# Optimization experiments

Measured on AMD Instinct MI355X. Metric: run time of the kernel, lower is better.

Reference implementation:

```python
import jax, jax.numpy as jnp
import numpy as np

B, L, D, H = 2, 2048, 1024, 16
HD = D // H  # head dim = 64


def setup_inputs() -> dict:
    key = jax.random.key(0)
    ks = jax.random.split(key, 5)
    s = 1.0 / np.sqrt(D)
    return {
        "x": jax.random.normal(ks[0], (B, L, D), dtype=jnp.float32),
        "mask": jnp.ones((B, 1, 1, L), dtype=jnp.int32),
        "Wq": jax.random.normal(ks[1], (D, D), dtype=jnp.float32) * s,
        "bq": jnp.zeros((D,), dtype=jnp.float32),
        "Wk": jax.random.normal(ks[2], (D, D), dtype=jnp.float32) * s,
        "bk": jnp.zeros((D,), dtype=jnp.float32),
        "Wv": jax.random.normal(ks[3], (D, D), dtype=jnp.float32) * s,
        "bv": jnp.zeros((D,), dtype=jnp.float32),
        "Wo": jax.random.normal(ks[4], (D, D), dtype=jnp.float32) * s,
        "bo": jnp.zeros((D,), dtype=jnp.float32),
    }


def reference(x, mask, Wq, bq, Wk, bk, Wv, bv, Wo, bo):
    Bx, Lx = x.shape[0], x.shape[1]
    # torch nn.Linear: y = x @ W.T + b
    q = (jnp.einsum("bld,ed->ble", x, Wq) + bq).reshape(Bx, Lx, H, HD).transpose(0, 2, 1, 3)
    k = (jnp.einsum("bld,ed->ble", x, Wk) + bk).reshape(Bx, Lx, H, HD).transpose(0, 2, 1, 3)
    v = (jnp.einsum("bld,ed->ble", x, Wv) + bv).reshape(Bx, Lx, H, HD).transpose(0, 2, 1, 3)
    # [B, H, L, L] scores
    scores = jnp.einsum("bhqd,bhkd->bhqk", q, k) / np.sqrt(HD).astype(np.float32)
    # faithful to original: masked positions are set to the tiny value 1e-9 (not -inf)
    scores = jnp.where(mask == 0, jnp.float32(1e-9), scores)
    attn = jax.nn.softmax(scores, axis=-1)
    # dropout_prob=0.0 -> identity (eval mode)
    out = jnp.einsum("bhqk,bhkd->bhqd", attn, v)  # [B, H, L, HD]
    out = out.transpose(0, 2, 1, 3).reshape(Bx, Lx, D)
    return jnp.einsum("bld,ed->ble", out, Wo) + bo
```

## Files before the change

kernel.cpp:

```cpp
#include <hip/hip_runtime.h>
#include <hip/hip_bf16.h>

typedef _Float16 f16;
typedef _Float16 f16x8 __attribute__((ext_vector_type(8)));
typedef _Float16 f16x4 __attribute__((ext_vector_type(4)));
typedef float f32x4 __attribute__((ext_vector_type(4)));
typedef int i32x4 __attribute__((ext_vector_type(4)));

#define LDS_LOAD16(gptr, lptr)                                                             \
  __builtin_amdgcn_global_load_lds(                                                        \
      (const __attribute__((address_space(1))) unsigned int*)(gptr),                       \
      (__attribute__((address_space(3))) unsigned int*)(lptr), 16, 0, 0)

#define ALPHA 0.18033688f
#define MASKVAL 1.44269504e-9f

__global__ __launch_bounds__(256) void conv_all(const float* __restrict__ x,
                                                const float* __restrict__ Wq,
                                                const float* __restrict__ Wk,
                                                const float* __restrict__ Wv,
                                                const float* __restrict__ Wo,
                                                f16* __restrict__ xh, f16* __restrict__ wqh,
                                                f16* __restrict__ wkh, f16* __restrict__ wvh,
                                                f16* __restrict__ woh) {
  int i = blockIdx.x * 256 + threadIdx.x;
  const float* src;
  f16* dst;
  int off;
  if (i < 524288) {
    src = x; dst = xh; off = i;
  } else {
    int j = i - 524288;
    int w = j >> 17;
    off = j & 131071;
    src = (w == 0) ? Wq : (w == 1) ? Wk : (w == 2) ? Wv : Wo;
    dst = (w == 0) ? wqh : (w == 1) ? wkh : (w == 2) ? wvh : woh;
  }
  const float4* s4 = (const float4*)src;
  float4 a = s4[2 * off];
  float4 b = s4[2 * off + 1];
  f16x8 o = {(f16)a.x, (f16)a.y, (f16)a.z, (f16)a.w,
             (f16)b.x, (f16)b.y, (f16)b.z, (f16)b.w};
  *(f16x8*)(dst + (size_t)off * 8) = o;
}

__global__ __launch_bounds__(256) void gemm_qkv(const f16* __restrict__ A,
                                                const f16* __restrict__ W0,
                                                const f16* __restrict__ W1,
                                                const f16* __restrict__ W2,
                                                const float* __restrict__ b0,
                                                const float* __restrict__ b1,
                                                const float* __restrict__ b2,
                                                f16* __restrict__ qo, f16* __restrict__ ko,
                                                f16* __restrict__ vo) {
  constexpr int K = 1024, BM = 128, BK = 32, NKT = K / BK;
  __shared__ f16 aT[2][BM * BK];
  __shared__ f16 bT[2][BM * BK];
  const int rid = (blockIdx.x & 7) * 96 + (blockIdx.x >> 3);
  const int z = rid >> 8;
  const f16* Bw = (z == 0) ? W0 : (z == 1) ? W1 : W2;
  const float* bias = (z == 0) ? b0 : (z == 1) ? b1 : b2;
  const int tid = threadIdx.x, wid = tid >> 6, lane = tid & 63;
  const int mb = ((rid >> 3) & 31) * BM, nb = (rid & 7) * BM;
  const int wr = wid >> 1, wc = wid & 1;
  const int lr = lane & 15, hi = lane >> 4;

  f32x4 acc[4][4] = {};

  const int r0 = tid >> 2, s0 = tid & 3;
  const int ci1 = 256 + tid, r1 = ci1 >> 2, s1 = ci1 & 3;

#define STAGE_QKV(bb, kt)                                                                   \
  do {                                                                                      \
    const int kb_ = (kt) * BK;                                                              \
    LDS_LOAD16(A + (size_t)(mb + r0) * K + kb_ + s0 * 8, (char*)aT[bb] + wid * 1024);       \
    LDS_LOAD16(Bw + (size_t)(nb + r0) * K + kb_ + s0 * 8, (char*)bT[bb] + wid * 1024);      \
    LDS_LOAD16(A + (size_t)(mb + r1) * K + kb_ + s1 * 8, (char*)aT[bb] + 4096 + wid * 1024);\
    LDS_LOAD16(Bw + (size_t)(nb + r1) * K + kb_ + s1 * 8, (char*)bT[bb] + 4096 + wid * 1024);\
  } while (0)

  STAGE_QKV(0, 0);
  for (int kt = 0; kt < NKT; ++kt) {
    const int p = kt & 1;
    if (kt + 1 < NKT) {
      STAGE_QKV(p ^ 1, kt + 1);
      asm volatile("s_waitcnt vmcnt(4)" ::: "memory");
    } else {
      asm volatile("s_waitcnt vmcnt(0)" ::: "memory");
    }
    __builtin_amdgcn_s_barrier();

    f16x8 af[4], bf[4];
#pragma unroll
    for (int i = 0; i < 4; ++i) af[i] = *(const f16x8*)&aT[p][(wr * 64 + i * 16 + lr) * BK + hi * 8];
#pragma unroll
    for (int j = 0; j < 4; ++j) bf[j] = *(const f16x8*)&bT[p][(wc * 64 + j * 16 + lr) * BK + hi * 8];
    __builtin_amdgcn_s_setprio(1);
#pragma unroll
    for (int i = 0; i < 4; ++i)
#pragma unroll
      for (int j = 0; j < 4; ++j)
        acc[i][j] = __builtin_amdgcn_mfma_f32_16x16x32_f16(af[i], bf[j], acc[i][j], 0, 0, 0);
    __builtin_amdgcn_s_setprio(0);
    __builtin_amdgcn_s_barrier();
  }

  const float scale = (z == 0) ? ALPHA : 1.0f;
#pragma unroll
  for (int i = 0; i < 4; ++i) {
#pragma unroll
    for (int j = 0; j < 4; ++j) {
      const int row = mb + wr * 64 + i * 16 + hi * 4;
      const int col = nb + wc * 64 + j * 16 + lr;
      const float bv = bias[col];
      const int hh = col >> 6, dd = col & 63;
      if (z == 2) {
        const int bb = row >> 11, l = row & 2047;
        f16x4 v4;
#pragma unroll
        for (int r = 0; r < 4; ++r) v4[r] = (f16)(acc[i][j][r] + bv);
        *(f16x4*)(vo + ((((size_t)bb * 16 + hh) * 64 + dd) * 2048 + l)) = v4;
      } else {
        f16* o = z ? ko : qo;
#pragma unroll
        for (int r = 0; r < 4; ++r) {
          const int m2 = row + r;
          const int bb = m2 >> 11, l = m2 & 2047;
          o[((((size_t)bb * 16 + hh) * 2048 + l) * 64) + dd] = (f16)((acc[i][j][r] + bv) * scale);
        }
      }
    }
  }
}

__global__ __launch_bounds__(256) void gemm_o(const f16* __restrict__ A,
                                              const f16* __restrict__ W,
                                              const float* __restrict__ bias,
                                              float* __restrict__ out) {
  constexpr int K = 1024, N = 1024, BK = 32, NKT = K / BK;
  __shared__ f16 aT[2][64 * BK];
  __shared__ f16 bT[2][128 * BK];
  const int rid = (blockIdx.x & 7) * 64 + (blockIdx.x >> 3);
  const int tid = threadIdx.x, wid = tid >> 6, lane = tid & 63;
  const int lr = lane & 15, hi = lane >> 4;
  const int mb = (rid >> 3) * 64, nb = (rid & 7) * 128;
  const int wr = wid >> 1, wc = wid & 1;
  f32x4 acc[2][4] = {};
  const int ra = tid >> 2, sa = tid & 3;
  const int rb1 = (256 + tid) >> 2, sb1 = (256 + tid) & 3;

#define STAGE_O(bb, kt)                                                                     \
  do {                                                                                      \
    const int kb_ = (kt) * BK;                                                              \
    LDS_LOAD16(A + (size_t)(mb + ra) * K + kb_ + sa * 8, (char*)aT[bb] + wid * 1024);       \
    LDS_LOAD16(W + (size_t)(nb + ra) * K + kb_ + sa * 8, (char*)bT[bb] + wid * 1024);       \
    LDS_LOAD16(W + (size_t)(nb + rb1) * K + kb_ + sb1 * 8, (char*)bT[bb] + 4096 + wid * 1024);\
  } while (0)

  STAGE_O(0, 0);
  for (int kt = 0; kt < NKT; ++kt) {
    const int p = kt & 1;
    if (kt + 1 < NKT) {
      STAGE_O(p ^ 1, kt + 1);
      asm volatile("s_waitcnt vmcnt(3)" ::: "memory");
    } else {
      asm volatile("s_waitcnt vmcnt(0)" ::: "memory");
    }
    __builtin_amdgcn_s_barrier();
    f16x8 af[2], bf[4];
#pragma unroll
    for (int i = 0; i < 2; ++i) af[i] = *(const f16x8*)&aT[p][(wr * 32 + i * 16 + lr) * BK + hi * 8];
#pragma unroll
    for (int j = 0; j < 4; ++j) bf[j] = *(const f16x8*)&bT[p][(wc * 64 + j * 16 + lr) * BK + hi * 8];
    __builtin_amdgcn_s_setprio(1);
#pragma unroll
    for (int i = 0; i < 2; ++i)
#pragma unroll
      for (int j = 0; j < 4; ++j)
        acc[i][j] = __builtin_amdgcn_mfma_f32_16x16x32_f16(af[i], bf[j], acc[i][j], 0, 0, 0);
    __builtin_amdgcn_s_setprio(0);
    __builtin_amdgcn_s_barrier();
  }
#pragma unroll
  for (int i = 0; i < 2; ++i)
#pragma unroll
    for (int j = 0; j < 4; ++j) {
      const int col = nb + wc * 64 + j * 16 + lr;
      const float bv = bias[col];
#pragma unroll
      for (int r = 0; r < 4; ++r)
        out[(size_t)(mb + wr * 32 + i * 16 + hi * 4 + r) * N + col] = acc[i][j][r] + bv;
    }
}

__global__ __launch_bounds__(256, 4) void attn4w(const f16* __restrict__ Qh,
                                                 const f16* __restrict__ Kh,
                                                 const f16* __restrict__ Vt,
                                                 const int* __restrict__ mask,
                                                 f16* __restrict__ Oa) {
  constexpr int L = 2048, HD = 64, H = 16, NT = L / 64;
  __shared__ __align__(16) char ldsb[32768];

  const int tid = threadIdx.x, w = tid >> 6, lane = tid & 63;
  const int lr = lane & 15, hi = lane >> 4;
  const int sw = lr & 7;

  const int bid = blockIdx.x;
  const int head = (bid & 7) * 4 + (bid >> 8);
  const int qb = (bid >> 3) & 31;
  const int b = head >> 4, h = head & 15;
  const int qr0 = qb * 64 + w * 16;

  const f16* Qb = Qh + (size_t)head * L * HD;
  const f16* Kb = Kh + (size_t)head * L * HD;
  const f16* Vb = Vt + (size_t)head * HD * L;
  const int* mrow = mask + b * L;

  int mred = 1;
  {
    const int4* m4 = (const int4*)mrow;
#pragma unroll
    for (int j = 0; j < 8; ++j) {
      int4 v = m4[lane + j * 64];
      mred &= v.x & v.y & v.z & v.w;
    }
  }
  const bool allm = __all(mred == 1);

  const int srow = lane >> 3;
  const int schk = (lane & 7) ^ srow;

#define STAGE4W(bb, kt)                                                                     \
  _Pragma("unroll") for (int c = 0; c < 2; ++c) {                                           \
    LDS_LOAD16(Kb + (size_t)((kt) * 64 + w * 16 + c * 8 + srow) * HD + schk * 8,            \
               ldsb + (bb) * 16384 + w * 2048 + c * 1024);                                  \
    LDS_LOAD16(Vb + (size_t)(w * 16 + c * 8 + srow) * L + (kt) * 64 + schk * 8,             \
               ldsb + (bb) * 16384 + 8192 + w * 2048 + c * 1024);                           \
  }

  const char* kbase0 = ldsb + lr * 128 + ((hi ^ sw) * 16);
  const char* kbase1 = ldsb + lr * 128 + (((4 + hi) ^ sw) * 16);

  f16x8 qf[2];
#pragma unroll
  for (int k2 = 0; k2 < 2; ++k2)
    qf[k2] = *(const f16x8*)&Qb[(size_t)(qr0 + lr) * HD + k2 * 32 + hi * 8];

  f32x4 oacc[4] = {};
  f32x4 lacc = {};
  const f32x4 zacc = {0.f, 0.f, 0.f, 0.f};
  const f16x8 ones = {1, 1, 1, 1, 1, 1, 1, 1};

  int4 mvA[4], mvB[4];
  if (!allm) {
#pragma unroll
    for (int nf = 0; nf < 4; ++nf) mvA[nf] = *(const int4*)&mrow[nf * 16 + hi * 4];
  }
  STAGE4W(0, 0);

#define ATTN_ITER(kt, P, MVR, MVL)                                                          \
  do {                                                                                      \
    asm volatile("s_waitcnt vmcnt(0)" ::: "memory");                                        \
    __builtin_amdgcn_s_barrier();                                                           \
    if ((kt) + 1 < NT) {                                                                    \
      if (!allm) {                                                                          \
        _Pragma("unroll") for (int nf = 0; nf < 4; ++nf)                                    \
            MVL[nf] = *(const int4*)&mrow[((kt) + 1) * 64 + nf * 16 + hi * 4];              \
      }                                                                                     \
      STAGE4W((P) ^ 1, (kt) + 1);                                                           \
    }                                                                                       \
    f16x8 kf[4][2];                                                                         \
    _Pragma("unroll") for (int nf = 0; nf < 4; ++nf) {                                      \
      kf[nf][0] = *(const f16x8*)(kbase0 + (P) * 16384 + nf * 2048);                        \
      kf[nf][1] = *(const f16x8*)(kbase1 + (P) * 16384 + nf * 2048);                        \
    }                                                                                       \
    f32x4 s[4];                                                                             \
    __builtin_amdgcn_s_setprio(1);                                                          \
    _Pragma("unroll") for (int nf = 0; nf < 4; ++nf) {                                      \
      f32x4 z = __builtin_amdgcn_mfma_f32_16x16x32_f16(kf[nf][0], qf[0], zacc, 0, 0, 0);    \
      s[nf] = __builtin_amdgcn_mfma_f32_16x16x32_f16(kf[nf][1], qf[1], z, 0, 0, 0);         \
    }                                                                                       \
    __builtin_amdgcn_s_setprio(0);                                                          \
    int wpk[4][2];                                                                          \
    _Pragma("unroll") for (int nf = 0; nf < 4; ++nf) {                                      \
      float p0, p1, p2, p3;                                                                 \
      if (allm) {                                                                           \
        p0 = __builtin_amdgcn_exp2f(s[nf][0]);                                              \
        p1 = __builtin_amdgcn_exp2f(s[nf][1]);                                              \
        p2 = __builtin_amdgcn_exp2f(s[nf][2]);                                              \
        p3 = __builtin_amdgcn_exp2f(s[nf][3]);                                              \
      } else {                                                                              \
        p0 = __builtin_amdgcn_exp2f(MVR[nf].x ? s[nf][0] : MASKVAL);                        \
        p1 = __builtin_amdgcn_exp2f(MVR[nf].y ? s[nf][1] : MASKVAL);                        \
        p2 = __builtin_amdgcn_exp2f(MVR[nf].z ? s[nf][2] : MASKVAL);                        \
        p3 = __builtin_amdgcn_exp2f(MVR[nf].w ? s[nf][3] : MASKVAL);                        \
      }                                                                                     \
      wpk[nf][0] = __builtin_bit_cast(int, __builtin_amdgcn_cvt_pkrtz(p0, p1));             \
      wpk[nf][1] = __builtin_bit_cast(int, __builtin_amdgcn_cvt_pkrtz(p2, p3));             \
    }                                                                                       \
    f16x8 pf[2];                                                                            \
    _Pragma("unroll") for (int k2 = 0; k2 < 2; ++k2) {                                      \
      int A0 = wpk[2 * k2][0], B0 = wpk[2 * k2 + 1][0];                                     \
      int A1 = wpk[2 * k2][1], B1 = wpk[2 * k2 + 1][1];                                     \
      asm("v_permlane32_swap_b32 %0, %1" : "+v"(A0), "+v"(B0));                             \
      asm("v_permlane16_swap_b32 %0, %1" : "+v"(A0), "+v"(B0));                             \
      asm("v_permlane32_swap_b32 %0, %1" : "+v"(A1), "+v"(B1));                             \
      asm("v_permlane16_swap_b32 %0, %1" : "+v"(A1), "+v"(B1));                             \
      i32x4 cc = {A0, A1, B0, B1};                                                          \
      pf[k2] = __builtin_bit_cast(f16x8, cc);                                               \
    }                                                                                       \
    __builtin_amdgcn_s_setprio(1);                                                          \
    _Pragma("unroll") for (int k2 = 0; k2 < 2; ++k2) {                                      \
      const char* vbase = (k2 ? kbase1 : kbase0) + (P) * 16384 + 8192;                      \
      _Pragma("unroll") for (int df = 0; df < 4; ++df) {                                    \
        f16x8 vf = *(const f16x8*)(vbase + df * 2048);                                      \
        oacc[df] = __builtin_amdgcn_mfma_f32_16x16x32_f16(pf[k2], vf, oacc[df], 0, 0, 0);   \
      }                                                                                     \
      lacc = __builtin_amdgcn_mfma_f32_16x16x32_f16(pf[k2], ones, lacc, 0, 0, 0);           \
    }                                                                                       \
    __builtin_amdgcn_s_setprio(0);                                                          \
  } while (0)

  for (int kt = 0; kt < NT; kt += 2) {
    ATTN_ITER(kt, 0, mvA, mvB);
    ATTN_ITER(kt + 1, 1, mvB, mvA);
  }

  f32x4 rinv;
#pragma unroll
  for (int r = 0; r < 4; ++r) rinv[r] = 1.0f / lacc[r];
#pragma unroll
  for (int df = 0; df < 4; ++df)
#pragma unroll
    for (int r = 0; r < 4; ++r) {
      const int l = qr0 + hi * 4 + r;
      Oa[(((size_t)b * L + l) * H + h) * HD + df * 16 + lr] = (f16)(oacc[df][r] * rinv[r]);
    }
}

extern "C" void kernel_launch(void* const* d_in, const int* in_sizes, int n_in,
                              void* d_out, int out_size, void* d_ws, size_t ws_size,
                              hipStream_t stream) {
  const float* x  = (const float*)d_in[0];
  const int* mask = (const int*)d_in[1];
  const float* Wq = (const float*)d_in[2];
  const float* bq = (const float*)d_in[3];
  const float* Wk = (const float*)d_in[4];
  const float* bk = (const float*)d_in[5];
  const float* Wv = (const float*)d_in[6];
  const float* bv = (const float*)d_in[7];
  const float* Wo = (const float*)d_in[8];
  const float* bo = (const float*)d_in[9];
  float* out = (float*)d_out;

  char* ws = (char*)d_ws;
  const size_t MB = 1u << 20;
  f16* xh  = (f16*)(ws);
  f16* wqh = (f16*)(ws + 8 * MB);
  f16* wkh = (f16*)(ws + 10 * MB);
  f16* wvh = (f16*)(ws + 12 * MB);
  f16* woh = (f16*)(ws + 14 * MB);
  f16* qh  = (f16*)(ws + 16 * MB);
  f16* kh  = (f16*)(ws + 24 * MB);
  f16* vth = (f16*)(ws + 32 * MB);
  f16* oah = (f16*)(ws + 40 * MB);

  conv_all<<<4096, 256, 0, stream>>>(x, Wq, Wk, Wv, Wo, xh, wqh, wkh, wvh, woh);

  gemm_qkv<<<768, 256, 0, stream>>>(xh, wqh, wkh, wvh, bq, bk, bv, qh, kh, vth);

  attn4w<<<dim3(1024), 256, 0, stream>>>(qh, kh, vth, mask, oah);

  gemm_o<<<512, 256, 0, stream>>>(oah, woh, bo, out);
}
```

Baseline: 117.3 us.

## Switch attention to 32x32x16 MFMA with 32 query rows per wave

The attention kernel now uses 32x32x16 MFMA tiles with 32 query rows per wave and 128 per block, halving the grid to 512 blocks. Each K/V LDS tile is reused across twice as many query rows, so there is half as much staging traffic per query. The row sum is now accumulated with scalar adds plus one cross-lane shuffle instead of an extra ones-MFMA, and fewer permlane swaps are needed. The costs are more registers (launch bounds drop to 2 blocks per SM) and fewer blocks, which may hurt occupancy and latency hiding.

```diff
diff --git a/kernel.cpp b/kernel.cpp
--- a/kernel.cpp
+++ b/kernel.cpp
@@ -5,6 +5,7 @@
 typedef _Float16 f16x8 __attribute__((ext_vector_type(8)));
 typedef _Float16 f16x4 __attribute__((ext_vector_type(4)));
 typedef float f32x4 __attribute__((ext_vector_type(4)));
+typedef float f32x16 __attribute__((ext_vector_type(16)));
 typedef int i32x4 __attribute__((ext_vector_type(4)));
 
 #define LDS_LOAD16(gptr, lptr)                                                             \
@@ -193,23 +194,22 @@
     }
 }
 
-__global__ __launch_bounds__(256, 4) void attn4w(const f16* __restrict__ Qh,
-                                                 const f16* __restrict__ Kh,
-                                                 const f16* __restrict__ Vt,
-                                                 const int* __restrict__ mask,
-                                                 f16* __restrict__ Oa) {
+__global__ __launch_bounds__(256, 2) void attn32q(const f16* __restrict__ Qh,
+                                                  const f16* __restrict__ Kh,
+                                                  const f16* __restrict__ Vt,
+                                                  const int* __restrict__ mask,
+                                                  f16* __restrict__ Oa) {
   constexpr int L = 2048, HD = 64, H = 16, NT = L / 64;
   __shared__ __align__(16) char ldsb[32768];
 
   const int tid = threadIdx.x, w = tid >> 6, lane = tid & 63;
-  const int lr = lane & 15, hi = lane >> 4;
-  const int sw = lr & 7;
+  const int q32 = lane & 31, h5 = lane >> 5, x7 = lane & 7;
 
   const int bid = blockIdx.x;
-  const int head = (bid & 7) * 4 + (bid >> 8);
-  const int qb = (bid >> 3) & 31;
+  const int head = (bid & 7) * 4 + (bid >> 7);
+  const int qb = (bid >> 3) & 15;
   const int b = head >> 4, h = head & 15;
-  const int qr0 = qb * 64 + w * 16;
+  const int qr0 = qb * 128 + w * 32;
 
   const f16* Qb = Qh + (size_t)head * L * HD;
   const f16* Kb = Kh + (size_t)head * L * HD;
@@ -230,7 +230,7 @@
   const int srow = lane >> 3;
   const int schk = (lane & 7) ^ srow;
 
-#define STAGE4W(bb, kt)                                                                     \
+#define STAGE32(bb, kt)                                                                     \
   _Pragma("unroll") for (int c = 0; c < 2; ++c) {                                           \
     LDS_LOAD16(Kb + (size_t)((kt) * 64 + w * 16 + c * 8 + srow) * HD + schk * 8,            \
                ldsb + (bb) * 16384 + w * 2048 + c * 1024);                                  \
@@ -238,103 +238,103 @@
                ldsb + (bb) * 16384 + 8192 + w * 2048 + c * 1024);                           \
   }
 
-  const char* kbase0 = ldsb + lr * 128 + ((hi ^ sw) * 16);
-  const char* kbase1 = ldsb + lr * 128 + (((4 + hi) ^ sw) * 16);
-
-  f16x8 qf[2];
-#pragma unroll
-  for (int k2 = 0; k2 < 2; ++k2)
-    qf[k2] = *(const f16x8*)&Qb[(size_t)(qr0 + lr) * HD + k2 * 32 + hi * 8];
-
-  f32x4 oacc[4] = {};
-  f32x4 lacc = {};
-  const f32x4 zacc = {0.f, 0.f, 0.f, 0.f};
-  const f16x8 ones = {1, 1, 1, 1, 1, 1, 1, 1};
-
-  int4 mvA[4], mvB[4];
+  const char* kb[4];
+#pragma unroll
+  for (int s = 0; s < 4; ++s)
+    kb[s] = ldsb + q32 * 128 + (((2 * s + h5) ^ x7) * 16);
+
+  f16x8 qf[4];
+#pragma unroll
+  for (int s = 0; s < 4; ++s)
+    qf[s] = *(const f16x8*)&Qb[(size_t)(qr0 + q32) * HD + s * 16 + h5 * 8];
+
+  f32x16 oacc[2] = {};
+  float lsum = 0.f;
+  const f32x16 zacc = {};
+
+  int4 mvA[2][4], mvB[2][4];
   if (!allm) {
 #pragma unroll
-    for (int nf = 0; nf < 4; ++nf) mvA[nf] = *(const int4*)&mrow[nf * 16 + hi * 4];
-  }
-  STAGE4W(0, 0);
-
-#define ATTN_ITER(kt, P, MVR, MVL)                                                          \
+    for (int t = 0; t < 2; ++t)
+#pragma unroll
+      for (int g = 0; g < 4; ++g) mvA[t][g] = *(const int4*)&mrow[t * 32 + 4 * h5 + 8 * g];
+  }
+  STAGE32(0, 0);
+
+#define ATTN_I32(kt, P, MVR, MVL)                                                           \
   do {                                                                                      \
     asm volatile("s_waitcnt vmcnt(0)" ::: "memory");                                        \
     __builtin_amdgcn_s_barrier();                                                           \
     if ((kt) + 1 < NT) {                                                                    \
       if (!allm) {                                                                          \
-        _Pragma("unroll") for (int nf = 0; nf < 4; ++nf)                                    \
-            MVL[nf] = *(const int4*)&mrow[((kt) + 1) * 64 + nf * 16 + hi * 4];              \
+        _Pragma("unroll") for (int t = 0; t < 2; ++t)                                       \
+            _Pragma("unroll") for (int g = 0; g < 4; ++g)                                   \
+                MVL[t][g] = *(const int4*)&mrow[((kt) + 1) * 64 + t * 32 + 4 * h5 + 8 * g]; \
       }                                                                                     \
-      STAGE4W((P) ^ 1, (kt) + 1);                                                           \
+      STAGE32((P) ^ 1, (kt) + 1);                                                           \
     }                                                                                       \
-    f16x8 kf[4][2];                                                                         \
-    _Pragma("unroll") for (int nf = 0; nf < 4; ++nf) {                                      \
-      kf[nf][0] = *(const f16x8*)(kbase0 + (P) * 16384 + nf * 2048);                        \
-      kf[nf][1] = *(const f16x8*)(kbase1 + (P) * 16384 + nf * 2048);                        \
-    }                                                                                       \
-    f32x4 s[4];                                                                             \
+    f32x16 st[2];                                                                           \
     __builtin_amdgcn_s_setprio(1);                                                          \
-    _Pragma("unroll") for (int nf = 0; nf < 4; ++nf) {                                      \
-      f32x4 z = __builtin_amdgcn_mfma_f32_16x16x32_f16(kf[nf][0], qf[0], zacc, 0, 0, 0);    \
-      s[nf] = __builtin_amdgcn_mfma_f32_16x16x32_f16(kf[nf][1], qf[1], z, 0, 0, 0);         \
+    _Pragma("unroll") for (int t = 0; t < 2; ++t) {                                         \
+      f32x16 a_ = zacc;                                                                     \
+      _Pragma("unroll") for (int s = 0; s < 4; ++s) {                                       \
+        f16x8 kf = *(const f16x8*)(kb[s] + (P) * 16384 + t * 4096);                         \
+        a_ = __builtin_amdgcn_mfma_f32_32x32x16_f16(kf, qf[s], a_, 0, 0, 0);                \
+      }                                                                                     \
+      st[t] = a_;                                                                           \
     }                                                                                       \
     __builtin_amdgcn_s_setprio(0);                                                          \
-    int wpk[4][2];                                                                          \
-    _Pragma("unroll") for (int nf = 0; nf < 4; ++nf) {                                      \
-      float p0, p1, p2, p3;                                                                 \
+    int u[2][8];                                                                            \
+    _Pragma("unroll") for (int t = 0; t < 2; ++t)                                           \
+        _Pragma("unroll") for (int j = 0; j < 8; ++j) {                                     \
+      float e0, e1;                                                                         \
       if (allm) {                                                                           \
-        p0 = __builtin_amdgcn_exp2f(s[nf][0]);                                              \
-        p1 = __builtin_amdgcn_exp2f(s[nf][1]);                                              \
-        p2 = __builtin_amdgcn_exp2f(s[nf][2]);                                              \
-        p3 = __builtin_amdgcn_exp2f(s[nf][3]);                                              \
+        e0 = __builtin_amdgcn_exp2f(st[t][2 * j]);                                          \
+        e1 = __builtin_amdgcn_exp2f(st[t][2 * j + 1]);                                      \
       } else {                                                                              \
-        p0 = __builtin_amdgcn_exp2f(MVR[nf].x ? s[nf][0] : MASKVAL);                        \
-        p1 = __builtin_amdgcn_exp2f(MVR[nf].y ? s[nf][1] : MASKVAL);                        \
-        p2 = __builtin_amdgcn_exp2f(MVR[nf].z ? s[nf][2] : MASKVAL);                        \
-        p3 = __builtin_amdgcn_exp2f(MVR[nf].w ? s[nf][3] : MASKVAL);                        \
+        const int r0_ = 2 * j, r1_ = 2 * j + 1;                                             \
+        int m0 = ((const int*)&MVR[t][r0_ >> 2])[r0_ & 3];                                  \
+        int m1 = ((const int*)&MVR[t][r1_ >> 2])[r1_ & 3];                                  \
+        e0 = __builtin_amdgcn_exp2f(m0 ? st[t][r0_] : MASKVAL);                             \
+        e1 = __builtin_amdgcn_exp2f(m1 ? st[t][r1_] : MASKVAL);                             \
       }                                                                                     \
-      wpk[nf][0] = __builtin_bit_cast(int, __builtin_amdgcn_cvt_pkrtz(p0, p1));             \
-      wpk[nf][1] = __builtin_bit_cast(int, __builtin_amdgcn_cvt_pkrtz(p2, p3));             \
-    }                                                                                       \
-    f16x8 pf[2];                                                                            \
-    _Pragma("unroll") for (int k2 = 0; k2 < 2; ++k2) {                                      \
-      int A0 = wpk[2 * k2][0], B0 = wpk[2 * k2 + 1][0];                                     \
-      int A1 = wpk[2 * k2][1], B1 = wpk[2 * k2 + 1][1];                                     \
-      asm("v_permlane32_swap_b32 %0, %1" : "+v"(A0), "+v"(B0));                             \
-      asm("v_permlane16_swap_b32 %0, %1" : "+v"(A0), "+v"(B0));                             \
-      asm("v_permlane32_swap_b32 %0, %1" : "+v"(A1), "+v"(B1));                             \
-      asm("v_permlane16_swap_b32 %0, %1" : "+v"(A1), "+v"(B1));                             \
-      i32x4 cc = {A0, A1, B0, B1};                                                          \
-      pf[k2] = __builtin_bit_cast(f16x8, cc);                                               \
+      lsum += e0 + e1;                                                                      \
+      u[t][j] = __builtin_bit_cast(int, __builtin_amdgcn_cvt_pkrtz(e0, e1));                \
     }                                                                                       \
     __builtin_amdgcn_s_setprio(1);                                                          \
-    _Pragma("unroll") for (int k2 = 0; k2 < 2; ++k2) {                                      \
-      const char* vbase = (k2 ? kbase1 : kbase0) + (P) * 16384 + 8192;                      \
-      _Pragma("unroll") for (int df = 0; df < 4; ++df) {                                    \
-        f16x8 vf = *(const f16x8*)(vbase + df * 2048);                                      \
-        oacc[df] = __builtin_amdgcn_mfma_f32_16x16x32_f16(pf[k2], vf, oacc[df], 0, 0, 0);   \
+    _Pragma("unroll") for (int t = 0; t < 2; ++t)                                           \
+        _Pragma("unroll") for (int sg = 0; sg < 2; ++sg) {                                  \
+      int X0 = u[t][sg * 4 + 0], Y0 = u[t][sg * 4 + 2];                                     \
+      int X1 = u[t][sg * 4 + 1], Y1 = u[t][sg * 4 + 3];                                     \
+      asm("v_permlane32_swap_b32 %0, %1" : "+v"(X0), "+v"(Y0));                             \
+      asm("v_permlane32_swap_b32 %0, %1" : "+v"(X1), "+v"(Y1));                             \
+      i32x4 cc = {X0, X1, Y0, Y1};                                                          \
+      f16x8 pfr = __builtin_bit_cast(f16x8, cc);                                            \
+      const int sp = t * 2 + sg;                                                            \
+      _Pragma("unroll") for (int dt = 0; dt < 2; ++dt) {                                    \
+        f16x8 vf = *(const f16x8*)(kb[sp] + (P) * 16384 + 8192 + dt * 4096);                \
+        oacc[dt] = __builtin_amdgcn_mfma_f32_32x32x16_f16(vf, pfr, oacc[dt], 0, 0, 0);      \
       }                                                                                     \
-      lacc = __builtin_amdgcn_mfma_f32_16x16x32_f16(pf[k2], ones, lacc, 0, 0, 0);           \
     }                                                                                       \
     __builtin_amdgcn_s_setprio(0);                                                          \
   } while (0)
 
   for (int kt = 0; kt < NT; kt += 2) {
-    ATTN_ITER(kt, 0, mvA, mvB);
-    ATTN_ITER(kt + 1, 1, mvB, mvA);
-  }
-
-  f32x4 rinv;
-#pragma unroll
-  for (int r = 0; r < 4; ++r) rinv[r] = 1.0f / lacc[r];
-#pragma unroll
-  for (int df = 0; df < 4; ++df)
-#pragma unroll
-    for (int r = 0; r < 4; ++r) {
-      const int l = qr0 + hi * 4 + r;
-      Oa[(((size_t)b * L + l) * H + h) * HD + df * 16 + lr] = (f16)(oacc[df][r] * rinv[r]);
+    ATTN_I32(kt, 0, mvA, mvB);
+    ATTN_I32(kt + 1, 1, mvB, mvA);
+  }
+
+  lsum += __shfl_xor(lsum, 32);
+  const float rinv = 1.0f / lsum;
+#pragma unroll
+  for (int dt = 0; dt < 2; ++dt)
+#pragma unroll
+    for (int g = 0; g < 4; ++g) {
+      f16x4 v4;
+#pragma unroll
+      for (int c = 0; c < 4; ++c) v4[c] = (f16)(oacc[dt][g * 4 + c] * rinv);
+      const int d0 = dt * 32 + 4 * h5 + 8 * g;
+      *(f16x4*)&Oa[(((size_t)b * L + qr0 + q32) * H + h) * HD + d0] = v4;
     }
 }
 
@@ -369,7 +369,7 @@
 
   gemm_qkv<<<768, 256, 0, stream>>>(xh, wqh, wkh, wvh, bq, bk, bv, qh, kh, vth);
 
-  attn4w<<<dim3(1024), 256, 0, stream>>>(qh, kh, vth, mask, oah);
+  attn32q<<<dim3(512), 256, 0, stream>>>(qh, kh, vth, mask, oah);
 
   gemm_o<<<512, 256, 0, stream>>>(oah, woh, bo, out);
 }
```

Result: no change. 117.2 us (-0.1%).

## Store V pre-swizzled in MFMA fragment order and load directly into registers

Applied to the files above, without the earlier changes.

The QKV GEMM epilogue now writes V into a per-64-key-tile layout that matches the lane and element order of the attention PV MFMA B-operand. The attention kernel then loads V fragments straight from global memory into registers each iteration instead of staging them through LDS, which halves the LDS footprint and removes the V LDS reads. The V global loads are issued after the barrier in the same iteration they are used, so their latency is less hidden than with the prefetched double-buffer. All four waves of a block also load the same V data redundantly.

```diff
diff --git a/kernel.cpp b/kernel.cpp
--- a/kernel.cpp
+++ b/kernel.cpp
@@ -116,10 +116,15 @@
       const int hh = col >> 6, dd = col & 63;
       if (z == 2) {
         const int bb = row >> 11, l = row & 2047;
+        const int head2 = bb * 16 + hh;
+        const int kvt = l & 63;
+        const int frag = (kvt >> 5) * 4 + j;
+        const int lane2 = ((kvt >> 3) & 3) * 16 + lr;
+        const int e0 = kvt & 7;
         f16x4 v4;
 #pragma unroll
         for (int r = 0; r < 4; ++r) v4[r] = (f16)(acc[i][j][r] + bv);
-        *(f16x4*)(vo + ((((size_t)bb * 16 + hh) * 64 + dd) * 2048 + l)) = v4;
+        *(f16x4*)&vo[(size_t)(head2 * 32 + (l >> 6)) * 4096 + frag * 512 + lane2 * 8 + e0] = v4;
       } else {
         f16* o = z ? ko : qo;
 #pragma unroll
@@ -195,11 +200,11 @@
 
 __global__ __launch_bounds__(256, 4) void attn4w(const f16* __restrict__ Qh,
                                                  const f16* __restrict__ Kh,
-                                                 const f16* __restrict__ Vt,
+                                                 const f16* __restrict__ Vf,
                                                  const int* __restrict__ mask,
                                                  f16* __restrict__ Oa) {
   constexpr int L = 2048, HD = 64, H = 16, NT = L / 64;
-  __shared__ __align__(16) char ldsb[32768];
+  __shared__ __align__(16) char ldsb[16384];
 
   const int tid = threadIdx.x, w = tid >> 6, lane = tid & 63;
   const int lr = lane & 15, hi = lane >> 4;
@@ -213,7 +218,7 @@
 
   const f16* Qb = Qh + (size_t)head * L * HD;
   const f16* Kb = Kh + (size_t)head * L * HD;
-  const f16* Vb = Vt + (size_t)head * HD * L;
+  const f16* Vb = Vf + (size_t)head * 32 * 4096;
   const int* mrow = mask + b * L;
 
   int mred = 1;
@@ -230,12 +235,10 @@
   const int srow = lane >> 3;
   const int schk = (lane & 7) ^ srow;
 
-#define STAGE4W(bb, kt)                                                                     \
+#define STAGE_K(bb, kt)                                                                     \
   _Pragma("unroll") for (int c = 0; c < 2; ++c) {                                           \
     LDS_LOAD16(Kb + (size_t)((kt) * 64 + w * 16 + c * 8 + srow) * HD + schk * 8,            \
-               ldsb + (bb) * 16384 + w * 2048 + c * 1024);                                  \
-    LDS_LOAD16(Vb + (size_t)(w * 16 + c * 8 + srow) * L + (kt) * 64 + schk * 8,             \
-               ldsb + (bb) * 16384 + 8192 + w * 2048 + c * 1024);                           \
+               ldsb + (bb) * 8192 + w * 2048 + c * 1024);                                   \
   }
 
   const char* kbase0 = ldsb + lr * 128 + ((hi ^ sw) * 16);
@@ -256,23 +259,29 @@
 #pragma unroll
     for (int nf = 0; nf < 4; ++nf) mvA[nf] = *(const int4*)&mrow[nf * 16 + hi * 4];
   }
-  STAGE4W(0, 0);
+  STAGE_K(0, 0);
 
 #define ATTN_ITER(kt, P, MVR, MVL)                                                          \
   do {                                                                                      \
     asm volatile("s_waitcnt vmcnt(0)" ::: "memory");                                        \
     __builtin_amdgcn_s_barrier();                                                           \
+                 \
+    f16x8 vreg[2][4];                                                                       \
+    _Pragma("unroll") for (int k2 = 0; k2 < 2; ++k2)                                        \
+        _Pragma("unroll") for (int df = 0; df < 4; ++df)                                    \
+            vreg[k2][df] = *(const f16x8*)&Vb[(size_t)(kt) * 4096 + (k2 * 4 + df) * 512 +   \
+                                              lane * 8];                                    \
     if ((kt) + 1 < NT) {                                                                    \
       if (!allm) {                                                                          \
         _Pragma("unroll") for (int nf = 0; nf < 4; ++nf)                                    \
             MVL[nf] = *(const int4*)&mrow[((kt) + 1) * 64 + nf * 16 + hi * 4];              \
       }                                                                                     \
-      STAGE4W((P) ^ 1, (kt) + 1);                                                           \
+      STAGE_K((P) ^ 1, (kt) + 1);                                                           \
     }                                                                                       \
     f16x8 kf[4][2];                                                                         \
     _Pragma("unroll") for (int nf = 0; nf < 4; ++nf) {                                      \
-      kf[nf][0] = *(const f16x8*)(kbase0 + (P) * 16384 + nf * 2048);                        \
-      kf[nf][1] = *(const f16x8*)(kbase1 + (P) * 16384 + nf * 2048);                        \
+      kf[nf][0] = *(const f16x8*)(kbase0 + (P) * 8192 + nf * 2048);                         \
+      kf[nf][1] = *(const f16x8*)(kbase1 + (P) * 8192 + nf * 2048);                         \
     }                                                                                       \
     f32x4 s[4];                                                                             \
     __builtin_amdgcn_s_setprio(1);                                                          \
@@ -311,11 +320,8 @@
     }                                                                                       \
     __builtin_amdgcn_s_setprio(1);                                                          \
     _Pragma("unroll") for (int k2 = 0; k2 < 2; ++k2) {                                      \
-      const char* vbase = (k2 ? kbase1 : kbase0) + (P) * 16384 + 8192;                      \
-      _Pragma("unroll") for (int df = 0; df < 4; ++df) {                                    \
-        f16x8 vf = *(const f16x8*)(vbase + df * 2048);                                      \
-        oacc[df] = __builtin_amdgcn_mfma_f32_16x16x32_f16(pf[k2], vf, oacc[df], 0, 0, 0);   \
-      }                                                                                     \
+      _Pragma("unroll") for (int df = 0; df < 4; ++df)                                      \
+          oacc[df] = __builtin_amdgcn_mfma_f32_16x16x32_f16(pf[k2], vreg[k2][df], oacc[df], 0, 0, 0); \
       lacc = __builtin_amdgcn_mfma_f32_16x16x32_f16(pf[k2], ones, lacc, 0, 0, 0);           \
     }                                                                                       \
     __builtin_amdgcn_s_setprio(0);                                                          \
@@ -362,14 +368,14 @@
   f16* woh = (f16*)(ws + 14 * MB);
   f16* qh  = (f16*)(ws + 16 * MB);
   f16* kh  = (f16*)(ws + 24 * MB);
-  f16* vth = (f16*)(ws + 32 * MB);
+  f16* vfh = (f16*)(ws + 32 * MB);
   f16* oah = (f16*)(ws + 40 * MB);
 
   conv_all<<<4096, 256, 0, stream>>>(x, Wq, Wk, Wv, Wo, xh, wqh, wkh, wvh, woh);
 
-  gemm_qkv<<<768, 256, 0, stream>>>(xh, wqh, wkh, wvh, bq, bk, bv, qh, kh, vth);
-
-  attn4w<<<dim3(1024), 256, 0, stream>>>(qh, kh, vth, mask, oah);
+  gemm_qkv<<<768, 256, 0, stream>>>(xh, wqh, wkh, wvh, bq, bk, bv, qh, kh, vfh);
+
+  attn4w<<<dim3(1024), 256, 0, stream>>>(qh, kh, vfh, mask, oah);
 
   gemm_o<<<512, 256, 0, stream>>>(oah, woh, bo, out);
 }
```

New measurement: 124.1 us. 5.8% more time.
